# Optimization experiments

Hardware: AMD Instinct MI355X
Metric: run time of the kernel (lower is better)

The kernel has to match this reference:

```python
import jax, jax.numpy as jnp
import numpy as np

B, V, N, E, F = 32, 6, 128, 128, 128  # batch, visits(=6), neighbour_size, ninfeat, noutfeat
NREL = 11
ALPHA = 0.2  # LeakyReLU negative slope


def setup_inputs() -> dict:
    key = jax.random.key(0)
    k1, k2, k3, k4, k5, k6 = jax.random.split(key, 6)
    feature_embed = jax.random.normal(k1, (B, V, N, E), dtype=jnp.float32)
    neighbour_embed = jax.random.normal(k2, (B, V, N, E), dtype=jnp.float32)
    w_index = jax.random.randint(k3, (B, V, N), 0, NREL + 1)
    # 0/1 keep mask, as in the original (indicator is a 01 tensor)
    indicator = (jax.random.uniform(k4, (B, V, N)) > 0.2).astype(jnp.float32)
    # stacked relation weight matrices, xavier_uniform with gain 1.414
    limit = 1.414 * np.sqrt(6.0 / (E + F))
    W = jax.random.uniform(k5, (NREL + 1, E, F), minval=-limit, maxval=limit, dtype=jnp.float32)
    # nn.Linear(2F, 1, bias=False) weight, stored transposed: (2F, 1)
    lim_a = 1.0 / np.sqrt(2 * F)
    a = jax.random.uniform(k6, (2 * F, 1), minval=-lim_a, maxval=lim_a, dtype=jnp.float32)
    return {"feature_embed": feature_embed, "neighbour_embed": neighbour_embed,
            "w_index": w_index, "indicator": indicator, "W": W, "a": a}


def reference(feature_embed, neighbour_embed, w_index, indicator, W, a):
    # gather per-edge relation weight matrices: (B,V,N,E,F)  -- the memory-heavy step
    Wg = W[w_index]
    neighbour = jnp.einsum('bvne,bvnef->bvnf', neighbour_embed, Wg)
    feature = jnp.einsum('bvne,bvnef->bvnf', feature_embed, Wg)
    hh = jnp.concatenate([neighbour, feature], axis=-1)           # (B,V,N,2F)
    e = jax.nn.leaky_relu(hh @ a, negative_slope=ALPHA)           # (B,V,N,1)
    attn = jax.nn.softmax(e, axis=-2)                             # softmax over neighbours
    # dropout is identity in eval mode
    attn = attn * indicator[..., None]                            # mask
    return jnp.einsum('bvnj,bvnf->bvf', attn, neighbour)          # (B,V,F)
```

## Files before the change

kernel.cpp:

```cpp
#include <hip/hip_runtime.h>

#define NREL1  12
#define NN     128
#define EE     128
#define FF     128
#define BV     192
#define RK     (NREL1 * EE)

#define WS_WA  0

__global__ __launch_bounds__(256) void prep_kernel(const float* __restrict__ W,
                                                   const float* __restrict__ a,
                                                   float* __restrict__ ws) {
    const int w    = blockIdx.x * 4 + (threadIdx.x >> 6);
    const int lane = threadIdx.x & 63;
    const int r = w >> 7, e = w & 127;
    const float2 wv = *(const float2*)(W + (size_t)(r * EE + e) * FF + lane * 2);
    const float2 a1 = *(const float2*)(a + lane * 2);
    const float2 a2 = *(const float2*)(a + FF + lane * 2);
    float d1 = wv.x * a1.x + wv.y * a1.y;
    float d2 = wv.x * a2.x + wv.y * a2.y;
#pragma unroll
    for (int off = 32; off; off >>= 1) {
        d1 += __shfl_xor(d1, off);
        d2 += __shfl_xor(d2, off);
    }
    if (lane == 0) {
        ws[WS_WA + r * EE + e]      = d1;
        ws[WS_WA + RK + r * EE + e] = d2;
    }
}

__global__ __launch_bounds__(1024) void gat_fused(const float* __restrict__ fe,
                                                  const float* __restrict__ ne,
                                                  const int* __restrict__ widx,
                                                  const float* __restrict__ ind,
                                                  const float* __restrict__ W,
                                                  const float* __restrict__ ws_r,
                                                  float* __restrict__ out) {
    __shared__ float wa[2 * RK];
    __shared__ float s16[16][RK];
    __shared__ float red[32][FF];
    __shared__ float red2[4][FF];
    __shared__ float e_lds[NN];
    __shared__ float attn_s[NN];
    __shared__ int   idx[NN];

    const int bv   = blockIdx.x;
    const int tid  = threadIdx.x;
    const int wave = tid >> 6;
    const int lane = tid & 63;
    const int l32  = lane & 31;
    const int half = lane >> 5;

    const float* ne_bv = ne + (size_t)bv * NN * EE;
    const float* fe_bv = fe + (size_t)bv * NN * EE;

    if (tid < NN) idx[tid] = widx[bv * NN + tid];

    float4 xr[8];
    {
        const float* base = (half ? fe_bv : ne_bv) + l32 * 4;
#pragma unroll
        for (int i = 0; i < 8; ++i)
            xr[i] = *(const float4*)(base + (wave * 8 + i) * EE);
    }

    if (tid < 2 * RK / 4)
        ((float4*)wa)[tid] = ((const float4*)(ws_r + WS_WA))[tid];
    {
        const float4 z = {0.f, 0.f, 0.f, 0.f};
#pragma unroll
        for (int q = 0; q < 6; ++q)
            ((float4*)&s16[0][0])[q * 1024 + tid] = z;
    }
    __syncthreads();

#pragma unroll
    for (int i = 0; i < 8; ++i) {
        const int n = wave * 8 + i;
        const int r = idx[n];
        const float4 wq = *(const float4*)&wa[half * RK + r * EE + l32 * 4];
        float d = xr[i].x * wq.x + xr[i].y * wq.y + xr[i].z * wq.z + xr[i].w * wq.w;
#pragma unroll
        for (int off = 32; off; off >>= 1) d += __shfl_xor(d, off);
        if (lane == 0) e_lds[n] = d > 0.f ? d : 0.2f * d;
    }
    __syncthreads();

    if (tid < 64) {
        float v0 = e_lds[tid], v1 = e_lds[tid + 64];
        float m = fmaxf(v0, v1);
#pragma unroll
        for (int off = 32; off; off >>= 1) m = fmaxf(m, __shfl_xor(m, off));
        float ex0 = expf(v0 - m), ex1 = expf(v1 - m);
        float ssum = ex0 + ex1;
#pragma unroll
        for (int off = 32; off; off >>= 1) ssum += __shfl_xor(ssum, off);
        float inv = 1.f / ssum;
        attn_s[tid]      = ex0 * inv * ind[bv * NN + tid];
        attn_s[tid + 64] = ex1 * inv * ind[bv * NN + tid + 64];
    }
    __syncthreads();

    if (half == 0) {
        float* sc = s16[wave];
#pragma unroll
        for (int i = 0; i < 8; ++i) {
            const int n = wave * 8 + i;
            const float an = attn_s[n];
            float* p = sc + idx[n] * EE + l32 * 4;
            float4 cur = *(const float4*)p;
            cur.x += an * xr[i].x; cur.y += an * xr[i].y;
            cur.z += an * xr[i].z; cur.w += an * xr[i].w;
            *(float4*)p = cur;
        }
    }
    __syncthreads();

    if (tid < RK / 4) {
        float4 v = *(const float4*)&s16[0][tid * 4];
#pragma unroll
        for (int c = 1; c < 16; ++c) {
            const float4 t = *(const float4*)&s16[c][tid * 4];
            v.x += t.x; v.y += t.y; v.z += t.z; v.w += t.w;
        }
        *(float4*)&s16[0][tid * 4] = v;
    }
    __syncthreads();

    {
        const int fq = tid & 31;
        const int kg = tid >> 5;
        float4 acc = {0.f, 0.f, 0.f, 0.f};
        const float* Wp = W + (size_t)(kg * 48) * FF + fq * 4;
        const float* Sp = &s16[0][kg * 48];
#pragma unroll 4
        for (int j = 0; j < 48; ++j) {
            const float sv = Sp[j];
            const float4 w4 = *(const float4*)(Wp + (size_t)j * FF);
            acc.x += sv * w4.x; acc.y += sv * w4.y;
            acc.z += sv * w4.z; acc.w += sv * w4.w;
        }
        *(float4*)&red[kg][fq * 4] = acc;
    }
    __syncthreads();
    if (tid < 512) {
        const int f = tid & 127, h = tid >> 7;
        float v = 0.f;
#pragma unroll
        for (int j = 0; j < 8; ++j) v += red[h * 8 + j][f];
        red2[h][f] = v;
    }
    __syncthreads();
    if (tid < FF)
        out[bv * FF + tid] = red2[0][tid] + red2[1][tid] + red2[2][tid] + red2[3][tid];
}

extern "C" void kernel_launch(void* const* d_in, const int* in_sizes, int n_in,
                              void* d_out, int out_size, void* d_ws, size_t ws_size,
                              hipStream_t stream) {
    const float* fe  = (const float*)d_in[0];
    const float* ne  = (const float*)d_in[1];
    const int*   wi  = (const int*)d_in[2];
    const float* ind = (const float*)d_in[3];
    const float* W   = (const float*)d_in[4];
    const float* a   = (const float*)d_in[5];
    float* out = (float*)d_out;
    float* ws  = (float*)d_ws;

    prep_kernel<<<RK / 4, 256, 0, stream>>>(W, a, ws);
    gat_fused<<<BV, 1024, 0, stream>>>(fe, ne, wi, ind, W, ws, out);
}
```

Measured before the change: 26.34 us.

## Replace per-wave scatter buffers with shared atomics and redundant per-wave softmax

New measurement: 44.52 us. +69.0%, slower.

```diff
diff --git a/kernel.cpp b/kernel.cpp
--- a/kernel.cpp
+++ b/kernel.cpp
@@ -39,93 +39,73 @@
                                                   const float* __restrict__ ws_r,
                                                   float* __restrict__ out) {
     __shared__ float wa[2 * RK];
-    __shared__ float s16[16][RK];
+    __shared__ float s1[RK];
     __shared__ float red[32][FF];
     __shared__ float red2[4][FF];
     __shared__ float e_lds[NN];
-    __shared__ float attn_s[NN];
     __shared__ int   idx[NN];
 
     const int bv   = blockIdx.x;
     const int tid  = threadIdx.x;
     const int wave = tid >> 6;
     const int lane = tid & 63;
-    const int l32  = lane & 31;
-    const int half = lane >> 5;
 
     const float* ne_bv = ne + (size_t)bv * NN * EE;
     const float* fe_bv = fe + (size_t)bv * NN * EE;
 
     if (tid < NN) idx[tid] = widx[bv * NN + tid];
 
-    float4 xr[8];
-    {
-        const float* base = (half ? fe_bv : ne_bv) + l32 * 4;
+    float2 xn[8], xf[8];
 #pragma unroll
-        for (int i = 0; i < 8; ++i)
-            xr[i] = *(const float4*)(base + (wave * 8 + i) * EE);
+    for (int i = 0; i < 8; ++i) {
+        const int n = wave * 8 + i;
+        xn[i] = *(const float2*)(ne_bv + (size_t)n * EE + lane * 2);
+        xf[i] = *(const float2*)(fe_bv + (size_t)n * EE + lane * 2);
     }
 
     if (tid < 2 * RK / 4)
         ((float4*)wa)[tid] = ((const float4*)(ws_r + WS_WA))[tid];
-    {
-        const float4 z = {0.f, 0.f, 0.f, 0.f};
-#pragma unroll
-        for (int q = 0; q < 6; ++q)
-            ((float4*)&s16[0][0])[q * 1024 + tid] = z;
-    }
+    if (tid < RK / 4)
+        ((float4*)s1)[tid] = make_float4(0.f, 0.f, 0.f, 0.f);
     __syncthreads();
 
 #pragma unroll
     for (int i = 0; i < 8; ++i) {
         const int n = wave * 8 + i;
         const int r = idx[n];
-        const float4 wq = *(const float4*)&wa[half * RK + r * EE + l32 * 4];
-        float d = xr[i].x * wq.x + xr[i].y * wq.y + xr[i].z * wq.z + xr[i].w * wq.w;
+        const float2 w1 = *(const float2*)&wa[r * EE + lane * 2];
+        const float2 w2 = *(const float2*)&wa[RK + r * EE + lane * 2];
+        float d = xn[i].x * w1.x + xn[i].y * w1.y
+                + xf[i].x * w2.x + xf[i].y * w2.y;
 #pragma unroll
         for (int off = 32; off; off >>= 1) d += __shfl_xor(d, off);
         if (lane == 0) e_lds[n] = d > 0.f ? d : 0.2f * d;
     }
     __syncthreads();
 
-    if (tid < 64) {
-        float v0 = e_lds[tid], v1 = e_lds[tid + 64];
+    float a0, a1;
+    {
+        const float v0 = e_lds[lane], v1 = e_lds[lane + 64];
         float m = fmaxf(v0, v1);
 #pragma unroll
         for (int off = 32; off; off >>= 1) m = fmaxf(m, __shfl_xor(m, off));
-        float ex0 = expf(v0 - m), ex1 = expf(v1 - m);
-        float ssum = ex0 + ex1;
+        const float ex0 = __expf(v0 - m), ex1 = __expf(v1 - m);
+        float ss = ex0 + ex1;
 #pragma unroll
-        for (int off = 32; off; off >>= 1) ssum += __shfl_xor(ssum, off);
-        float inv = 1.f / ssum;
-        attn_s[tid]      = ex0 * inv * ind[bv * NN + tid];
-        attn_s[tid + 64] = ex1 * inv * ind[bv * NN + tid + 64];
+        for (int off = 32; off; off >>= 1) ss += __shfl_xor(ss, off);
+        const float inv = 1.f / ss;
+        a0 = ex0 * inv * ind[bv * NN + lane];
+        a1 = ex1 * inv * ind[bv * NN + lane + 64];
     }
-    __syncthreads();
 
-    if (half == 0) {
-        float* sc = s16[wave];
 #pragma unroll
-        for (int i = 0; i < 8; ++i) {
-            const int n = wave * 8 + i;
-            const float an = attn_s[n];
-            float* p = sc + idx[n] * EE + l32 * 4;
-            float4 cur = *(const float4*)p;
-            cur.x += an * xr[i].x; cur.y += an * xr[i].y;
-            cur.z += an * xr[i].z; cur.w += an * xr[i].w;
-            *(float4*)p = cur;
-        }
-    }
-    __syncthreads();
-
-    if (tid < RK / 4) {
-        float4 v = *(const float4*)&s16[0][tid * 4];
-#pragma unroll
-        for (int c = 1; c < 16; ++c) {
-            const float4 t = *(const float4*)&s16[c][tid * 4];
-            v.x += t.x; v.y += t.y; v.z += t.z; v.w += t.w;
-        }
-        *(float4*)&s16[0][tid * 4] = v;
+    for (int i = 0; i < 8; ++i) {
+        const int n  = wave * 8 + i;
+        const float an = (wave < 8) ? __shfl(a0, n) : __shfl(a1, n - 64);
+        const int r  = idx[n];
+        float* p = &s1[r * EE + lane * 2];
+        atomicAdd(p + 0, an * xn[i].x);
+        atomicAdd(p + 1, an * xn[i].y);
     }
     __syncthreads();
 
@@ -134,7 +114,7 @@
         const int kg = tid >> 5;
         float4 acc = {0.f, 0.f, 0.f, 0.f};
         const float* Wp = W + (size_t)(kg * 48) * FF + fq * 4;
-        const float* Sp = &s16[0][kg * 48];
+        const float* Sp = &s1[kg * 48];
 #pragma unroll 4
         for (int j = 0; j < 48; ++j) {
             const float sv = Sp[j];
```
